# Kernel tuning notes

Measured on AMD Instinct MI355X. Metric: run time of the kernel, lower is better.

The kernel has to match this reference:

```python
import jax, jax.numpy as jnp
import numpy as np

NHID = 512
NCLS = 250
CHUNK = 200  # words per class (equal class_chunks), vocab = NCLS*CHUNK = 50000
N = 2048     # flattened tokens (batch*seq after masking)


def setup_inputs() -> dict:
    key = jax.random.key(0)
    k1, k2, k3, k4, k5 = jax.random.split(key, 5)
    r = 0.1  # init_weights uniform range
    x = jax.random.normal(k1, (N, NHID), dtype=jnp.float32)
    cls_idx = jax.random.randint(k2, (N,), 0, NCLS, dtype=jnp.int64)
    Wc = jax.random.uniform(k3, (NCLS, NHID), jnp.float32, -r, r)   # cls_decoder.weight
    bc = jnp.zeros((NCLS,), jnp.float32)                             # cls_decoder.bias
    Ww = jax.random.uniform(k4, (NCLS, CHUNK, NHID), jnp.float32, -r, r)  # stacked words_decoders weights
    bw = jnp.zeros((NCLS, CHUNK), jnp.float32)                       # stacked words_decoders biases
    return {"x": x, "Wc": Wc, "bc": bc, "Ww": Ww, "bw": bw, "cls_idx": cls_idx}


def reference(x, Wc, bc, Ww, bw, cls_idx):
    # Class logits for every token: cls_decoder(input)
    p_class = jnp.einsum('nh,ch->nc', x, Wc) + bc          # [N, NCLS]
    # Per-class word decoders: each token goes through the Linear of its class.
    # Equivalent to the dict-based index_select + per-class Linear in the
    # original forward (rows reordered per-token instead of grouped by class).
    Wg = Ww[cls_idx]                                       # [N, CHUNK, NHID] irregular gather
    bg = bw[cls_idx]                                       # [N, CHUNK]
    p_words = jnp.einsum('nkh,nh->nk', Wg, x) + bg         # [N, CHUNK]
    # Concatenate class and within-class logits into one array output.
    return jnp.concatenate([p_class, p_words], axis=1)     # [N, NCLS+CHUNK]
```

## Files before the change

kernel.cpp:

```cpp
#include <hip/hip_runtime.h>

#define NHID   512
#define NCLS   250
#define CHUNK  200
#define NTOK   2048
#define NOUT   450
#define NPAN   13
#define NWB    (NCLS * NPAN)
#define NCB    256
#define NBLK   (NWB + NCB)
#define NTHR   64
#define MAXTOK 64

typedef __attribute__((ext_vector_type(8))) short bf16x8;
typedef __attribute__((ext_vector_type(4))) float f32x4;

#define MFMA(a, b, c) __builtin_amdgcn_mfma_f32_16x16x32_bf16((a), (b), (c), 0, 0, 0)

__device__ __forceinline__ unsigned hpack(unsigned a, unsigned b) {
    return __builtin_amdgcn_perm(a, b, 0x07060302u);
}

__device__ __forceinline__ void cvt8(float4 va, float4 vb, bf16x8& h, bf16x8& l) {
    unsigned u0 = __float_as_uint(va.x), u1 = __float_as_uint(va.y);
    unsigned u2 = __float_as_uint(va.z), u3 = __float_as_uint(va.w);
    unsigned u4 = __float_as_uint(vb.x), u5 = __float_as_uint(vb.y);
    unsigned u6 = __float_as_uint(vb.z), u7 = __float_as_uint(vb.w);
    union { unsigned w[4]; bf16x8 v; } H, L;
    H.w[0] = hpack(u1, u0); H.w[1] = hpack(u3, u2);
    H.w[2] = hpack(u5, u4); H.w[3] = hpack(u7, u6);
    float r0 = va.x - __uint_as_float(u0 & 0xffff0000u);
    float r1 = va.y - __uint_as_float(u1 & 0xffff0000u);
    float r2 = va.z - __uint_as_float(u2 & 0xffff0000u);
    float r3 = va.w - __uint_as_float(u3 & 0xffff0000u);
    float r4 = vb.x - __uint_as_float(u4 & 0xffff0000u);
    float r5 = vb.y - __uint_as_float(u5 & 0xffff0000u);
    float r6 = vb.z - __uint_as_float(u6 & 0xffff0000u);
    float r7 = vb.w - __uint_as_float(u7 & 0xffff0000u);
    L.w[0] = hpack(__float_as_uint(r1), __float_as_uint(r0));
    L.w[1] = hpack(__float_as_uint(r3), __float_as_uint(r2));
    L.w[2] = hpack(__float_as_uint(r5), __float_as_uint(r4));
    L.w[3] = hpack(__float_as_uint(r7), __float_as_uint(r6));
    h = H.v; l = L.v;
}

__device__ __forceinline__ void lds_fence_wave() {
    __builtin_amdgcn_wave_barrier();
    asm volatile("s_waitcnt lgkmcnt(0)" ::: "memory");
    __builtin_amdgcn_wave_barrier();
}

__global__ __launch_bounds__(NTHR)
void cbd_fused(const float* __restrict__ x,  const float* __restrict__ Wc,
               const float* __restrict__ bc, const float* __restrict__ Ww,
               const float* __restrict__ bw, const int* __restrict__ cls_idx,
               float* __restrict__ out)
{
    const int bid  = blockIdx.x;
    const int lane = threadIdx.x;
    const int n    = lane & 15;
    const int q    = lane >> 4;

    if (bid >= NWB) {
        const int pcb = bid - NWB;
        const int mt = pcb >> 1, hn = pcb & 1;
        const float* ap = x + (size_t)(mt * 16 + n) * NHID + q * 8;
        #pragma unroll
        for (int g4 = 0; g4 < 2; ++g4) {
            const float* bp[4]; float bias[4]; int col[4]; bool rv[4];
            #pragma unroll
            for (int k = 0; k < 4; ++k) {
                int r = (hn * 8 + g4 * 4 + k) * 16 + n;
                rv[k] = r < NCLS;
                int rc = rv[k] ? r : NCLS - 1;
                bp[k]   = Wc + (size_t)rc * NHID + q * 8;
                bias[k] = bc[rc];
                col[k]  = rc;
            }
            f32x4 acc[4] = {{0,0,0,0},{0,0,0,0},{0,0,0,0},{0,0,0,0}};
            #pragma unroll 2
            for (int s = 0; s < 16; ++s) {
                float4 a0 = *(const float4*)(ap + s * 32);
                float4 a1 = *(const float4*)(ap + s * 32 + 4);
                bf16x8 ah, al; cvt8(a0, a1, ah, al);
                #pragma unroll
                for (int k = 0; k < 4; ++k) {
                    float4 b0 = *(const float4*)(bp[k] + s * 32);
                    float4 b1 = *(const float4*)(bp[k] + s * 32 + 4);
                    bf16x8 bh, bl; cvt8(b0, b1, bh, bl);
                    acc[k] = MFMA(ah, bh, acc[k]);
                    acc[k] = MFMA(al, bh, acc[k]);
                    acc[k] = MFMA(ah, bl, acc[k]);
                }
            }
            #pragma unroll
            for (int k = 0; k < 4; ++k)
                if (rv[k]) {
                    #pragma unroll
                    for (int i = 0; i < 4; ++i)
                        out[(size_t)(mt * 16 + q * 4 + i) * NOUT + col[k]]
                            = acc[k][i] + bias[k];
                }
        }
        return;
    }

    const int c = bid / NPAN;
    const int p = bid - c * NPAN;

    int myvals[32];
    #pragma unroll
    for (int it = 0; it < 8; ++it) {
        int4 v = *(const int4*)&cls_idx[it * 256 + lane * 4];
        myvals[it*4+0] = v.x; myvals[it*4+1] = v.y;
        myvals[it*4+2] = v.z; myvals[it*4+3] = v.w;
    }
    __shared__ int toktmp[MAXTOK];
    int cnt = 0;
    #pragma unroll
    for (int j = 0; j < 32; ++j) {
        int idx  = (j >> 2) * 256 + lane * 4 + (j & 3);
        bool hit = (myvals[j] == c);
        unsigned long long m = __ballot(hit);
        if (hit) {
            int pos = cnt + (int)__popcll(m & ((1ull << lane) - 1ull));
            if (pos < MAXTOK) toktmp[pos] = idx;
        }
        cnt += (int)__popcll(m);
    }
    if (cnt == 0) return;
    const int cntc = cnt < MAXTOK ? cnt : MAXTOK;
    lds_fence_wave();

    const int r  = p * 16 + n;
    const int rr = r < CHUNK ? r : CHUNK - 1;
    const float* wp  = Ww + ((size_t)c * CHUNK + rr) * NHID + q * 8;
    const float bias = bw[c * CHUNK + rr];

    for (int sb = 0; sb < cntc; sb += 16) {
        int slot  = sb + n;
        int mytok = toktmp[slot < cntc ? slot : 0];
        int tkS[4]; bool msk[4];
        #pragma unroll
        for (int i = 0; i < 4; ++i) {
            int m = q * 4 + i;
            tkS[i] = __shfl(mytok, m);
            msk[i] = (sb + m) < cntc;
        }
        const float* apx = x + (size_t)mytok * NHID + q * 8;

        f32x4 acc = {0.f, 0.f, 0.f, 0.f};
        #pragma unroll 4
        for (int s = 0; s < 16; ++s) {
            float4 a0 = *(const float4*)(apx + s * 32);
            float4 a1 = *(const float4*)(apx + s * 32 + 4);
            float4 b0 = *(const float4*)(wp + s * 32);
            float4 b1 = *(const float4*)(wp + s * 32 + 4);
            bf16x8 ah, al, bh, bl;
            cvt8(a0, a1, ah, al);
            cvt8(b0, b1, bh, bl);
            acc = MFMA(ah, bh, acc);
            acc = MFMA(al, bh, acc);
            acc = MFMA(ah, bl, acc);
        }

        if (r < CHUNK) {
            #pragma unroll
            for (int i = 0; i < 4; ++i)
                if (msk[i])
                    out[(size_t)tkS[i] * NOUT + NCLS + r] = acc[i] + bias;
        }
    }
}

extern "C" void kernel_launch(void* const* d_in, const int* in_sizes, int n_in,
                              void* d_out, int out_size, void* d_ws, size_t ws_size,
                              hipStream_t stream) {
    const float* x   = (const float*)d_in[0];
    const float* Wc  = (const float*)d_in[1];
    const float* bc  = (const float*)d_in[2];
    const float* Ww  = (const float*)d_in[3];
    const float* bw  = (const float*)d_in[4];
    const int*   cls = (const int*)d_in[5];
    float* out = (float*)d_out;
    hipLaunchKernelGGL(cbd_fused, dim3(NBLK), dim3(NTHR), 0, stream,
                       x, Wc, bc, Ww, bw, cls, out);
}
```

Measured before the change: 210.8 us.

## Software-pipeline global loads with register double buffering and reorder block roles

```diff
diff --git a/kernel.cpp b/kernel.cpp
--- a/kernel.cpp
+++ b/kernel.cpp
@@ -50,7 +50,7 @@
     __builtin_amdgcn_wave_barrier();
 }
 
-__global__ __launch_bounds__(NTHR)
+__global__ __launch_bounds__(NTHR, 3)
 void cbd_fused(const float* __restrict__ x,  const float* __restrict__ Wc,
                const float* __restrict__ bc, const float* __restrict__ Ww,
                const float* __restrict__ bw, const int* __restrict__ cls_idx,
@@ -61,9 +61,8 @@
     const int n    = lane & 15;
     const int q    = lane >> 4;
 
-    if (bid >= NWB) {
-        const int pcb = bid - NWB;
-        const int mt = pcb >> 1, hn = pcb & 1;
+    if (bid < NCB) {
+        const int mt = bid >> 1, hn = bid & 1;
         const float* ap = x + (size_t)(mt * 16 + n) * NHID + q * 8;
         #pragma unroll
         for (int g4 = 0; g4 < 2; ++g4) {
@@ -78,19 +77,36 @@
                 col[k]  = rc;
             }
             f32x4 acc[4] = {{0,0,0,0},{0,0,0,0},{0,0,0,0},{0,0,0,0}};
+            float4 qa[2][2], qb[2][8];
+            #pragma unroll
+            for (int j = 0; j < 2; ++j) {
+                qa[j][0] = *(const float4*)(ap + j * 32);
+                qa[j][1] = *(const float4*)(ap + j * 32 + 4);
+                #pragma unroll
+                for (int k = 0; k < 4; ++k) {
+                    qb[j][2*k]   = *(const float4*)(bp[k] + j * 32);
+                    qb[j][2*k+1] = *(const float4*)(bp[k] + j * 32 + 4);
+                }
+            }
             #pragma unroll 2
             for (int s = 0; s < 16; ++s) {
-                float4 a0 = *(const float4*)(ap + s * 32);
-                float4 a1 = *(const float4*)(ap + s * 32 + 4);
-                bf16x8 ah, al; cvt8(a0, a1, ah, al);
+                const int b = s & 1;
+                bf16x8 ah, al; cvt8(qa[b][0], qa[b][1], ah, al);
                 #pragma unroll
                 for (int k = 0; k < 4; ++k) {
-                    float4 b0 = *(const float4*)(bp[k] + s * 32);
-                    float4 b1 = *(const float4*)(bp[k] + s * 32 + 4);
-                    bf16x8 bh, bl; cvt8(b0, b1, bh, bl);
+                    bf16x8 bh, bl; cvt8(qb[b][2*k], qb[b][2*k+1], bh, bl);
                     acc[k] = MFMA(ah, bh, acc[k]);
                     acc[k] = MFMA(al, bh, acc[k]);
                     acc[k] = MFMA(ah, bl, acc[k]);
+                }
+                if (s + 2 < 16) {
+                    qa[b][0] = *(const float4*)(ap + (s+2) * 32);
+                    qa[b][1] = *(const float4*)(ap + (s+2) * 32 + 4);
+                    #pragma unroll
+                    for (int k = 0; k < 4; ++k) {
+                        qb[b][2*k]   = *(const float4*)(bp[k] + (s+2) * 32);
+                        qb[b][2*k+1] = *(const float4*)(bp[k] + (s+2) * 32 + 4);
+                    }
                 }
             }
             #pragma unroll
@@ -105,8 +121,22 @@
         return;
     }
 
-    const int c = bid / NPAN;
-    const int p = bid - c * NPAN;
+    const int wb = bid - NCB;
+    const int c = wb / NPAN;
+    const int p = wb - c * NPAN;
+
+    const int r  = p * 16 + n;
+    const int rr = r < CHUNK ? r : CHUNK - 1;
+    const float* wp = Ww + ((size_t)c * CHUNK + rr) * NHID + q * 8;
+
+    float4 pb[2][4];
+    #pragma unroll
+    for (int j = 0; j < 2; ++j)
+        #pragma unroll
+        for (int t = 0; t < 2; ++t) {
+            pb[j][2*t]   = *(const float4*)(wp + (2*j + t) * 32);
+            pb[j][2*t+1] = *(const float4*)(wp + (2*j + t) * 32 + 4);
+        }
 
     int myvals[32];
     #pragma unroll
@@ -132,9 +162,6 @@
     const int cntc = cnt < MAXTOK ? cnt : MAXTOK;
     lds_fence_wave();
 
-    const int r  = p * 16 + n;
-    const int rr = r < CHUNK ? r : CHUNK - 1;
-    const float* wp  = Ww + ((size_t)c * CHUNK + rr) * NHID + q * 8;
     const float bias = bw[c * CHUNK + rr];
 
     for (int sb = 0; sb < cntc; sb += 16) {
@@ -149,19 +176,47 @@
         }
         const float* apx = x + (size_t)mytok * NHID + q * 8;
 
+        float4 pa[2][4];
+        #pragma unroll
+        for (int j = 0; j < 2; ++j)
+            #pragma unroll
+            for (int t = 0; t < 2; ++t) {
+                pa[j][2*t]   = *(const float4*)(apx + (2*j + t) * 32);
+                pa[j][2*t+1] = *(const float4*)(apx + (2*j + t) * 32 + 4);
+            }
+        if (sb > 0) {
+            #pragma unroll
+            for (int j = 0; j < 2; ++j)
+                #pragma unroll
+                for (int t = 0; t < 2; ++t) {
+                    pb[j][2*t]   = *(const float4*)(wp + (2*j + t) * 32);
+                    pb[j][2*t+1] = *(const float4*)(wp + (2*j + t) * 32 + 4);
+                }
+        }
+
         f32x4 acc = {0.f, 0.f, 0.f, 0.f};
-        #pragma unroll 4
-        for (int s = 0; s < 16; ++s) {
-            float4 a0 = *(const float4*)(apx + s * 32);
-            float4 a1 = *(const float4*)(apx + s * 32 + 4);
-            float4 b0 = *(const float4*)(wp + s * 32);
-            float4 b1 = *(const float4*)(wp + s * 32 + 4);
-            bf16x8 ah, al, bh, bl;
-            cvt8(a0, a1, ah, al);
-            cvt8(b0, b1, bh, bl);
-            acc = MFMA(ah, bh, acc);
-            acc = MFMA(al, bh, acc);
-            acc = MFMA(ah, bl, acc);
+        #pragma unroll 2
+        for (int j = 0; j < 8; ++j) {
+            const int b = j & 1;
+            #pragma unroll
+            for (int t = 0; t < 2; ++t) {
+                bf16x8 ah, al, bh, bl;
+                cvt8(pa[b][2*t], pa[b][2*t+1], ah, al);
+                cvt8(pb[b][2*t], pb[b][2*t+1], bh, bl);
+                acc = MFMA(ah, bh, acc);
+                acc = MFMA(al, bh, acc);
+                acc = MFMA(ah, bl, acc);
+            }
+            if (j + 2 < 8) {
+                #pragma unroll
+                for (int t = 0; t < 2; ++t) {
+                    const int s = 2 * (j + 2) + t;
+                    pa[b][2*t]   = *(const float4*)(apx + s * 32);
+                    pa[b][2*t+1] = *(const float4*)(apx + s * 32 + 4);
+                    pb[b][2*t]   = *(const float4*)(wp + s * 32);
+                    pb[b][2*t+1] = *(const float4*)(wp + s * 32 + 4);
+                }
+            }
         }
 
         if (r < CHUNK) {
```

After: 174.4 us. -17.2%, faster.

## Restructure into one block per class with async LDS weight pipeline

Applied to the files above, without the earlier changes.

```diff
diff --git a/kernel.cpp b/kernel.cpp
--- a/kernel.cpp
+++ b/kernel.cpp
@@ -5,11 +5,9 @@
 #define CHUNK  200
 #define NTOK   2048
 #define NOUT   450
-#define NPAN   13
-#define NWB    (NCLS * NPAN)
-#define NCB    256
-#define NBLK   (NWB + NCB)
-#define NTHR   64
+#define NPANW  13
+#define NBLK   250
+#define NTHR   512
 #define MAXTOK 64
 
 typedef __attribute__((ext_vector_type(8))) short bf16x8;
@@ -44,10 +42,66 @@
     h = H.v; l = L.v;
 }
 
-__device__ __forceinline__ void lds_fence_wave() {
-    __builtin_amdgcn_wave_barrier();
-    asm volatile("s_waitcnt lgkmcnt(0)" ::: "memory");
-    __builtin_amdgcn_wave_barrier();
+__device__ __forceinline__ void async16(const float* g, float* lds_base) {
+    __builtin_amdgcn_global_load_lds(
+        (const __attribute__((address_space(1))) unsigned*)g,
+        (__attribute__((address_space(3))) unsigned*)lds_base, 16, 0, 0);
+}
+
+__device__ __forceinline__ void issue_quarter(const float* wbase, int P, int kq,
+                                              float* dst, int lane) {
+    #pragma unroll
+    for (int i = 0; i < 8; ++i) {
+        int j  = 2 * i + (lane >> 5);
+        int rj = P * 16 + j; if (rj > CHUNK - 1) rj = CHUNK - 1;
+        int sl = (lane & 31) ^ (j & 7);
+        async16(wbase + (size_t)rj * NHID + kq * 128 + sl * 4, dst + i * 256);
+    }
+}
+
+__device__ __forceinline__ void class_unit(int u, int wid, int lane, int n, int q,
+                                           const float* __restrict__ x,
+                                           const float* __restrict__ Wc,
+                                           const float* __restrict__ bc,
+                                           float* __restrict__ out) {
+    const int mt = u >> 1, hn = u & 1;
+    const int g4 = (wid >> 2) & 1, kk = wid & 3;
+    const int rC = (hn * 8 + g4 * 4 + kk) * 16 + n;
+    const bool rv = rC < NCLS;
+    const int  rc = rv ? rC : NCLS - 1;
+    const float* ap = x  + (size_t)(mt * 16 + n) * NHID + q * 8;
+    const float* bp = Wc + (size_t)rc * NHID + q * 8;
+    const float bias = bc[rc];
+    f32x4 acc = {0.f, 0.f, 0.f, 0.f};
+    float4 qa[2][2], qb[2][2];
+    #pragma unroll
+    for (int j = 0; j < 2; ++j) {
+        qa[j][0] = *(const float4*)(ap + j * 32);
+        qa[j][1] = *(const float4*)(ap + j * 32 + 4);
+        qb[j][0] = *(const float4*)(bp + j * 32);
+        qb[j][1] = *(const float4*)(bp + j * 32 + 4);
+    }
+    #pragma unroll 2
+    for (int s = 0; s < 16; ++s) {
+        const int b = s & 1;
+        bf16x8 ah, al, bh, bl;
+        cvt8(qa[b][0], qa[b][1], ah, al);
+        cvt8(qb[b][0], qb[b][1], bh, bl);
+        acc = MFMA(ah, bh, acc);
+        acc = MFMA(al, bh, acc);
+        acc = MFMA(ah, bl, acc);
+        if (s + 2 < 16) {
+            qa[b][0] = *(const float4*)(ap + (s + 2) * 32);
+            qa[b][1] = *(const float4*)(ap + (s + 2) * 32 + 4);
+            qb[b][0] = *(const float4*)(bp + (s + 2) * 32);
+            qb[b][1] = *(const float4*)(bp + (s + 2) * 32 + 4);
+        }
+    }
+    if (rv) {
+        #pragma unroll
+        for (int i = 0; i < 4; ++i)
+            out[(size_t)(mt * 16 + q * 4 + i) * NOUT + rc] = acc[i] + bias;
+    }
 }
 
 __global__ __launch_bounds__(NTHR)
@@ -56,57 +110,17 @@
                const float* __restrict__ bw, const int* __restrict__ cls_idx,
                float* __restrict__ out)
 {
-    const int bid  = blockIdx.x;
-    const int lane = threadIdx.x;
+    __shared__ float ringA[5][2][2048];
+    __shared__ float ringB[3][2048];
+    __shared__ short Afrag[16384];
+    __shared__ int   toktmp[MAXTOK];
+
+    const int tid  = threadIdx.x;
+    const int wid  = tid >> 6;
+    const int lane = tid & 63;
     const int n    = lane & 15;
     const int q    = lane >> 4;
-
-    if (bid >= NWB) {
-        const int pcb = bid - NWB;
-        const int mt = pcb >> 1, hn = pcb & 1;
-        const float* ap = x + (size_t)(mt * 16 + n) * NHID + q * 8;
-        #pragma unroll
-        for (int g4 = 0; g4 < 2; ++g4) {
-            const float* bp[4]; float bias[4]; int col[4]; bool rv[4];
-            #pragma unroll
-            for (int k = 0; k < 4; ++k) {
-                int r = (hn * 8 + g4 * 4 + k) * 16 + n;
-                rv[k] = r < NCLS;
-                int rc = rv[k] ? r : NCLS - 1;
-                bp[k]   = Wc + (size_t)rc * NHID + q * 8;
-                bias[k] = bc[rc];
-                col[k]  = rc;
-            }
-            f32x4 acc[4] = {{0,0,0,0},{0,0,0,0},{0,0,0,0},{0,0,0,0}};
-            #pragma unroll 2
-            for (int s = 0; s < 16; ++s) {
-                float4 a0 = *(const float4*)(ap + s * 32);
-                float4 a1 = *(const float4*)(ap + s * 32 + 4);
-                bf16x8 ah, al; cvt8(a0, a1, ah, al);
-                #pragma unroll
-                for (int k = 0; k < 4; ++k) {
-                    float4 b0 = *(const float4*)(bp[k] + s * 32);
-                    float4 b1 = *(const float4*)(bp[k] + s * 32 + 4);
-                    bf16x8 bh, bl; cvt8(b0, b1, bh, bl);
-                    acc[k] = MFMA(ah, bh, acc[k]);
-                    acc[k] = MFMA(al, bh, acc[k]);
-                    acc[k] = MFMA(ah, bl, acc[k]);
-                }
-            }
-            #pragma unroll
-            for (int k = 0; k < 4; ++k)
-                if (rv[k]) {
-                    #pragma unroll
-                    for (int i = 0; i < 4; ++i)
-                        out[(size_t)(mt * 16 + q * 4 + i) * NOUT + col[k]]
-                            = acc[k][i] + bias[k];
-                }
-        }
-        return;
-    }
-
-    const int c = bid / NPAN;
-    const int p = bid - c * NPAN;
+    const int c    = blockIdx.x;
 
     int myvals[32];
     #pragma unroll
@@ -115,7 +129,6 @@
         myvals[it*4+0] = v.x; myvals[it*4+1] = v.y;
         myvals[it*4+2] = v.z; myvals[it*4+3] = v.w;
     }
-    __shared__ int toktmp[MAXTOK];
     int cnt = 0;
     #pragma unroll
     for (int j = 0; j < 32; ++j) {
@@ -128,47 +141,117 @@
         }
         cnt += (int)__popcll(m);
     }
-    if (cnt == 0) return;
-    const int cntc = cnt < MAXTOK ? cnt : MAXTOK;
-    lds_fence_wave();
-
-    const int r  = p * 16 + n;
-    const int rr = r < CHUNK ? r : CHUNK - 1;
-    const float* wp  = Ww + ((size_t)c * CHUNK + rr) * NHID + q * 8;
-    const float bias = bw[c * CHUNK + rr];
-
-    for (int sb = 0; sb < cntc; sb += 16) {
-        int slot  = sb + n;
-        int mytok = toktmp[slot < cntc ? slot : 0];
-        int tkS[4]; bool msk[4];
+    const int cnt1 = cnt < 16 ? cnt : 16;
+
+    const int p0   = wid;
+    const int p1   = 8 + wid;
+    const int npan = (wid < 5) ? 2 : 1;
+
+    int tkS[4]; bool msk[4]; float bias0 = 0.f, bias1 = 0.f;
+    if (cnt) {
+        int mytokA = toktmp[n < cnt1 ? n : cnt1 - 1];
         #pragma unroll
         for (int i = 0; i < 4; ++i) {
-            int m = q * 4 + i;
-            tkS[i] = __shfl(mytok, m);
-            msk[i] = (sb + m) < cntc;
-        }
-        const float* apx = x + (size_t)mytok * NHID + q * 8;
+            tkS[i] = __shfl(mytokA, q * 4 + i);
+            msk[i] = (q * 4 + i) < cnt1;
+        }
+        { int rr = p0 * 16 + n; if (rr > CHUNK - 1) rr = CHUNK - 1;
+          bias0 = bw[c * CHUNK + rr]; }
+        if (npan == 2) {
+            int rr = p1 * 16 + n; if (rr > CHUNK - 1) rr = CHUNK - 1;
+            bias1 = bw[c * CHUNK + rr];
+        }
+        #pragma unroll
+        for (int rep = 0; rep < 2; ++rep) {
+            int job = tid * 2 + rep;
+            int tok = job >> 6, s = (job >> 2) & 15, qq = job & 3;
+            int ti  = toktmp[tok < cnt1 ? tok : cnt1 - 1];
+            const float* xp = x + (size_t)ti * NHID + s * 32 + qq * 8;
+            float4 a0 = *(const float4*)xp, a1 = *(const float4*)(xp + 4);
+            bf16x8 hh, ll; cvt8(a0, a1, hh, ll);
+            char* ab = (char*)Afrag + tok * 2048 + s * 128;
+            *(bf16x8*)(ab + (((qq * 2    ) ^ (tok & 7)) << 4)) = hh;
+            *(bf16x8*)(ab + (((qq * 2 + 1) ^ (tok & 7)) << 4)) = ll;
+        }
+    }
+    __syncthreads();
+
+    if (cnt) {
+        const float* wbase = Ww + (size_t)c * CHUNK * NHID;
+        float* rb0 = (wid < 5) ? &ringA[wid][0][0] : &ringB[wid - 5][0];
+        float* rb1 = (wid < 5) ? &ringA[wid][1][0] : rb0;
+        const int depth = (wid < 5) ? 2 : 1;
+        const int nQ    = npan * 4;
+
+        issue_quarter(wbase, p0, 0, rb0, lane);
+        if (depth == 2) issue_quarter(wbase, p0, 1, rb1, lane);
 
         f32x4 acc = {0.f, 0.f, 0.f, 0.f};
-        #pragma unroll 4
-        for (int s = 0; s < 16; ++s) {
-            float4 a0 = *(const float4*)(apx + s * 32);
-            float4 a1 = *(const float4*)(apx + s * 32 + 4);
-            float4 b0 = *(const float4*)(wp + s * 32);
-            float4 b1 = *(const float4*)(wp + s * 32 + 4);
-            bf16x8 ah, al, bh, bl;
-            cvt8(a0, a1, ah, al);
-            cvt8(b0, b1, bh, bl);
-            acc = MFMA(ah, bh, acc);
-            acc = MFMA(al, bh, acc);
-            acc = MFMA(ah, bl, acc);
-        }
-
-        if (r < CHUNK) {
+        for (int iq = 0; iq < nQ; ++iq) {
+            if (depth == 2 && iq != nQ - 1)
+                asm volatile("s_waitcnt vmcnt(8)" ::: "memory");
+            else
+                asm volatile("s_waitcnt vmcnt(0)" ::: "memory");
+
+            const int kq = iq & 3;
+            const float* qb = (depth == 2 && (iq & 1)) ? rb1 : rb0;
+            if (kq == 0) { acc[0]=0.f; acc[1]=0.f; acc[2]=0.f; acc[3]=0.f; }
+
             #pragma unroll
-            for (int i = 0; i < 4; ++i)
-                if (msk[i])
-                    out[(size_t)tkS[i] * NOUT + NCLS + r] = acc[i] + bias;
+            for (int t4 = 0; t4 < 4; ++t4) {
+                const int s = kq * 4 + t4;
+                const char* ab = (const char*)Afrag + n * 2048 + s * 128;
+                bf16x8 ah = *(const bf16x8*)(ab + (((q*2    ) ^ (n&7)) << 4));
+                bf16x8 al = *(const bf16x8*)(ab + (((q*2 + 1) ^ (n&7)) << 4));
+                const float* bp = qb + n * 128 + t4 * 32;
+                float4 b0 = *(const float4*)(bp + (((q*2    ) ^ (n&7)) << 2));
+                float4 b1 = *(const float4*)(bp + (((q*2 + 1) ^ (n&7)) << 2));
+                bf16x8 bh, bl; cvt8(b0, b1, bh, bl);
+                acc = MFMA(ah, bh, acc);
+                acc = MFMA(al, bh, acc);
+                acc = MFMA(ah, bl, acc);
+            }
+
+            if (kq == 3) {
+                const int   P = (iq >= 4) ? p1 : p0;
+                const int   r = P * 16 + n;
+                const float biasP = (iq >= 4) ? bias1 : bias0;
+                if (r < CHUNK) {
+                    #pragma unroll
+                    for (int i = 0; i < 4; ++i)
+                        if (msk[i])
+                            out[(size_t)tkS[i] * NOUT + NCLS + r] = acc[i] + biasP;
+                }
+            }
+
+            const int nx = iq + depth;
+            if (nx < nQ)
+                issue_quarter(wbase, (nx >= 4) ? p1 : p0, nx & 3,
+                              (depth == 2 && (nx & 1)) ? rb1 : rb0, lane);
+        }
+    }
+
+    class_unit(c, wid, lane, n, q, x, Wc, bc, out);
+    if (c < 6) class_unit(NCLS + c, wid, lane, n, q, x, Wc, bc, out);
+
+    if (cnt > 16) {
+        const int cw = cnt < MAXTOK ? cnt : MAXTOK;
+        const int ov = cw - 16;
+        for (int j = tid; j < ov * CHUNK; j += NTHR) {
+            const int g  = j / CHUNK;
+            const int rr = j - g * CHUNK;
+            const int ti = toktmp[16 + g];
+            const float4* wr = (const float4*)(Ww + ((size_t)c * CHUNK + rr) * NHID);
+            const float4* xr = (const float4*)(x + (size_t)ti * NHID);
+            float s0 = 0.f, s1 = 0.f, s2 = 0.f, s3 = 0.f;
+            #pragma unroll 4
+            for (int k = 0; k < 128; ++k) {
+                float4 a = wr[k], b = xr[k];
+                s0 += a.x * b.x; s1 += a.y * b.y;
+                s2 += a.z * b.z; s3 += a.w * b.w;
+            }
+            out[(size_t)ti * NOUT + NCLS + rr] =
+                (s0 + s1) + (s2 + s3) + bw[c * CHUNK + rr];
         }
     }
 }
```

After: 190.5 us. -9.6%, faster.
